# Kernel tuning notes

Measured on AMD Instinct MI355X. Metric: run time of the kernel, lower is better.

The kernel has to match this reference:

```python
import jax, jax.numpy as jnp
import numpy as np

SUBNET_NUM = 32
BATCH = 131072
H1, H2 = 10, 6          # subnet_arch = [10, 6]
SMOOTH_LAMBDA = 0.001
BN_EPS = 1e-10


def setup_inputs() -> dict:
    key = jax.random.key(0)
    ks = jax.random.split(key, 7)
    f32 = jnp.float32
    x = jax.random.normal(ks[0], (BATCH, SUBNET_NUM), f32)
    # small init scale keeps tanh in its non-saturated (smooth) regime
    W1 = 0.5 * jax.random.normal(ks[1], (SUBNET_NUM, 1, H1), f32)
    b1 = 0.1 * jax.random.normal(ks[2], (SUBNET_NUM, H1), f32)
    W2 = 0.5 * jax.random.normal(ks[3], (SUBNET_NUM, H1, H2), f32)
    b2 = 0.1 * jax.random.normal(ks[4], (SUBNET_NUM, H2), f32)
    W3 = 0.5 * jax.random.normal(ks[5], (SUBNET_NUM, H2, 1), f32)
    b3 = 0.1 * jax.random.normal(ks[6], (SUBNET_NUM, 1), f32)
    return {"x": x, "W1": W1, "b1": b1, "W2": W2, "b2": b2, "W3": W3, "b3": b3}


def _subnet_scalar(x_s, w1, b1, w2, b2, w3, b3):
    """One subnet applied to one scalar input: output and d2out/dx2."""
    def f(xs):
        h = jnp.tanh(xs * w1[0] + b1)        # [H1]  (input dim is 1)
        h = jnp.tanh(h @ w2 + b2)            # [H2]
        return (h @ w3)[0] + b3[0]           # scalar
    out = f(x_s)
    g2 = jax.grad(jax.grad(f))(x_s)          # second derivative wrt the scalar input
    return out, g2


def reference(x, W1, b1, W2, b2, W3, b3):
    # vmap over batch (inner) and over subnets (outer, axis 1 of x / axis 0 of params)
    per_batch = jax.vmap(_subnet_scalar, in_axes=(0, None, None, None, None, None, None))
    per_subnet = jax.vmap(per_batch, in_axes=(1, 0, 0, 0, 0, 0, 0), out_axes=(1, 1))
    out, g2 = per_subnet(x, W1, b1, W2, b2, W3, b3)      # each [BATCH, SUBNET_NUM]

    # BatchNorm (momentum=0.0, center=False, scale=False) in training mode:
    # normalize by batch stats; moving_variance == biased batch variance.
    mean = jnp.mean(out, axis=0)
    var = jnp.mean((out - mean) ** 2, axis=0)
    out_bn = (out - mean) * jax.lax.rsqrt(var + BN_EPS)

    # smooth penalty per subnet: mean(grad2^2) / sqrt(moving_variance)
    penalty = jnp.mean(g2 ** 2, axis=0) / jnp.sqrt(var)
    smooth_loss = SMOOTH_LAMBDA * jnp.sum(penalty)
    return out_bn, smooth_loss
```

## Files before the change

### kernel.cpp

```cpp
#include <hip/hip_runtime.h>

#define BATCH 131072
#define SN 32
#define H1 10
#define H2 6
#define TILE_ROWS 64
#define NBLK (BATCH / TILE_ROWS)
#define LDS_STRIDE 33

__device__ __forceinline__ float fast_tanh(float x) {
    float e = __expf(2.0f * x);
    float r = __builtin_amdgcn_rcpf(e + 1.0f);
    return fmaf(-2.0f, r, 1.0f);
}

__global__ __launch_bounds__(256) void k_main(
    const float* __restrict__ x,
    const float* __restrict__ W1, const float* __restrict__ B1,
    const float* __restrict__ W2, const float* __restrict__ B2,
    const float* __restrict__ W3, const float* __restrict__ B3,
    float* __restrict__ out, float* __restrict__ partial )
{
    __shared__ float xt[TILE_ROWS * LDS_STRIDE];
    const int tid = threadIdx.x;
    const int row0 = blockIdx.x * TILE_ROWS;

    const float4* xv = (const float4*)(x + (size_t)row0 * SN);
    #pragma unroll
    for (int it = 0; it < 2; ++it) {
        int v = it * 256 + tid;
        float4 val = xv[v];
        int r = v >> 3;
        int c = (v & 7) << 2;
        float* dst = &xt[r * LDS_STRIDE + c];
        dst[0] = val.x; dst[1] = val.y; dst[2] = val.z; dst[3] = val.w;
    }
    __syncthreads();

    const int lane = tid & 63;
    const int wave = tid >> 6;

    #pragma unroll 1
    for (int si = 0; si < SN / 4; ++si) {
        const int s = __builtin_amdgcn_readfirstlane(si * 4 + wave);
        const float* w1p = W1 + s * H1;
        const float* b1p = B1 + s * H1;
        const float* w2p = W2 + s * H1 * H2;
        const float* b2p = B2 + s * H2;
        const float* w3p = W3 + s * H2;
        const float b3 = B3[s];

        float w1r[H1], b1r[H1];
        #pragma unroll
        for (int i = 0; i < H1; ++i) { w1r[i] = w1p[i]; b1r[i] = b1p[i]; }
        float w2r[H1 * H2];
        #pragma unroll
        for (int k = 0; k < H1 * H2; ++k) w2r[k] = w2p[k];
        float b2r[H2], w3r[H2];
        #pragma unroll
        for (int j = 0; j < H2; ++j) { b2r[j] = b2p[j]; w3r[j] = w3p[j]; }

        const float xs = xt[lane * LDS_STRIDE + s];

        float t[H1], p[H1], q[H1];
        #pragma unroll
        for (int i = 0; i < H1; ++i) {
            float u = fmaf(xs, w1r[i], b1r[i]);
            float ti = fast_tanh(u);
            float e = fmaf(-ti, ti, 1.0f);
            t[i] = ti;
            p[i] = e * w1r[i];
            q[i] = -2.0f * ti * e * w1r[i] * w1r[i];
        }

        float outv = b3, g2 = 0.0f;
        #pragma unroll
        for (int j = 0; j < H2; ++j) {
            float v = b2r[j], a = 0.0f, c = 0.0f;
            #pragma unroll
            for (int i = 0; i < H1; ++i) {
                const float w = w2r[i * H2 + j];
                v = fmaf(w, t[i], v);
                a = fmaf(w, p[i], a);
                c = fmaf(w, q[i], c);
            }
            float sj = fast_tanh(v);
            float dj = fmaf(-sj, sj, 1.0f);
            float g2j = dj * c - 2.0f * sj * dj * a * a;
            outv = fmaf(w3r[j], sj, outv);
            g2   = fmaf(w3r[j], g2j, g2);
        }

        out[(size_t)(row0 + lane) * SN + s] = outv;

        float s1 = outv, s2 = outv * outv, s3 = g2 * g2;
        #pragma unroll
        for (int off = 32; off > 0; off >>= 1) {
            s1 += __shfl_xor(s1, off);
            s2 += __shfl_xor(s2, off);
            s3 += __shfl_xor(s3, off);
        }
        if (lane == 0) {
            partial[(size_t)(0 * SN + s) * NBLK + blockIdx.x] = s1;
            partial[(size_t)(1 * SN + s) * NBLK + blockIdx.x] = s2;
            partial[(size_t)(2 * SN + s) * NBLK + blockIdx.x] = s3;
        }
    }
}

__global__ __launch_bounds__(256) void k_reduce(const float* __restrict__ partial,
                                                double* __restrict__ acc)
{
    const float* p = partial + (size_t)blockIdx.x * NBLK;
    double s = 0.0;
    for (int i = threadIdx.x; i < NBLK; i += 256) s += (double)p[i];
    #pragma unroll
    for (int off = 32; off > 0; off >>= 1) s += __shfl_down(s, off);
    __shared__ double ws[4];
    if ((threadIdx.x & 63) == 0) ws[threadIdx.x >> 6] = s;
    __syncthreads();
    if (threadIdx.x == 0) acc[blockIdx.x] = ws[0] + ws[1] + ws[2] + ws[3];
}

__global__ __launch_bounds__(256) void k_norm(float* __restrict__ out,
                                              const double* __restrict__ acc)
{
    __shared__ float mean_s[SN], inv_s[SN];
    const int tid = threadIdx.x;
    if (tid < SN) {
        const double invB = 1.0 / (double)BATCH;
        double mean = acc[tid] * invB;
        double var = acc[SN + tid] * invB - mean * mean;
        if (var < 0.0) var = 0.0;
        mean_s[tid] = (float)mean;
        inv_s[tid] = (float)(1.0 / sqrt(var + 1e-10));
    }
    if (blockIdx.x == 0 && tid == 0) {
        const double invB = 1.0 / (double)BATCH;
        double sum = 0.0;
        for (int s = 0; s < SN; ++s) {
            double mean = acc[s] * invB;
            double var = acc[SN + s] * invB - mean * mean;
            if (var < 0.0) var = 0.0;
            sum += (acc[2 * SN + s] * invB) / sqrt(var);
        }
        out[(size_t)BATCH * SN] = (float)(0.001 * sum);
    }
    __syncthreads();
    const int v = blockIdx.x * 256 + tid;
    float4* p = (float4*)out;
    float4 val = p[v];
    const int c = (v & 7) << 2;
    val.x = (val.x - mean_s[c + 0]) * inv_s[c + 0];
    val.y = (val.y - mean_s[c + 1]) * inv_s[c + 1];
    val.z = (val.z - mean_s[c + 2]) * inv_s[c + 2];
    val.w = (val.w - mean_s[c + 3]) * inv_s[c + 3];
    p[v] = val;
}

extern "C" void kernel_launch(void* const* d_in, const int* in_sizes, int n_in,
                              void* d_out, int out_size, void* d_ws, size_t ws_size,
                              hipStream_t stream) {
    const float* x  = (const float*)d_in[0];
    const float* W1 = (const float*)d_in[1];
    const float* B1 = (const float*)d_in[2];
    const float* W2 = (const float*)d_in[3];
    const float* B2 = (const float*)d_in[4];
    const float* W3 = (const float*)d_in[5];
    const float* B3 = (const float*)d_in[6];

    float* out = (float*)d_out;
    float* partial = (float*)d_ws;
    double* acc = (double*)((char*)d_ws + (size_t)3 * SN * NBLK * sizeof(float));

    k_main<<<NBLK, 256, 0, stream>>>(x, W1, B1, W2, B2, W3, B3, out, partial);
    k_reduce<<<3 * SN, 256, 0, stream>>>(partial, acc);
    k_norm<<<(BATCH * SN / 4) / 256, 256, 0, stream>>>(out, acc);
}
```

Before: 139.5 us.

## Process two rows per lane with packed float2 math and stage outputs in LDS

Each lane now handles two batch rows using two-wide vector types, so the compiler can emit packed FP32 FMA instructions and amortize per-subnet weight loads over more rows; the tile grows to 128 rows per block. Outputs are staged in LDS and written as coalesced float4 stores instead of strided scalar stores. The second-derivative algebra is also refactored, folding the constant factor into a final multiply by 4. This adds register and LDS pressure, and the block count is halved.

```diff
diff --git a/kernel.cpp b/kernel.cpp
--- a/kernel.cpp
+++ b/kernel.cpp
@@ -4,14 +4,22 @@
 #define SN 32
 #define H1 10
 #define H2 6
-#define TILE_ROWS 64
-#define NBLK (BATCH / TILE_ROWS)
+#define ROWS 128
+#define GRID (BATCH / ROWS)
 #define LDS_STRIDE 33
 
-__device__ __forceinline__ float fast_tanh(float x) {
-    float e = __expf(2.0f * x);
-    float r = __builtin_amdgcn_rcpf(e + 1.0f);
-    return fmaf(-2.0f, r, 1.0f);
+typedef float v2f __attribute__((ext_vector_type(2)));
+
+__device__ __forceinline__ v2f bc(float s) { v2f r; r.x = s; r.y = s; return r; }
+__device__ __forceinline__ v2f fma2(v2f a, v2f b, v2f c) {
+    return __builtin_elementwise_fma(a, b, c);
+}
+__device__ __forceinline__ v2f tanh2(v2f x) {
+    v2f x2 = x + x;
+    v2f e; e.x = __expf(x2.x); e.y = __expf(x2.y);
+    v2f e1 = e + bc(1.0f);
+    v2f r; r.x = __builtin_amdgcn_rcpf(e1.x); r.y = __builtin_amdgcn_rcpf(e1.y);
+    return fma2(bc(-2.0f), r, bc(1.0f));
 }
 
 __global__ __launch_bounds__(256) void k_main(
@@ -21,13 +29,16 @@
     const float* __restrict__ W3, const float* __restrict__ B3,
     float* __restrict__ out, float* __restrict__ partial )
 {
-    __shared__ float xt[TILE_ROWS * LDS_STRIDE];
+    __shared__ float xt[ROWS * LDS_STRIDE];
+    __shared__ float ov[ROWS * LDS_STRIDE];
     const int tid = threadIdx.x;
-    const int row0 = blockIdx.x * TILE_ROWS;
-
-    const float4* xv = (const float4*)(x + (size_t)row0 * SN);
+    const int lane = tid & 63;
+    const int wave = tid >> 6;
+    const int blk = blockIdx.x;
+
+    const float4* xv = (const float4*)(x + (size_t)blk * ROWS * SN);
     #pragma unroll
-    for (int it = 0; it < 2; ++it) {
+    for (int it = 0; it < 4; ++it) {
         int v = it * 256 + tid;
         float4 val = xv[v];
         int r = v >> 3;
@@ -37,11 +48,8 @@
     }
     __syncthreads();
 
-    const int lane = tid & 63;
-    const int wave = tid >> 6;
-
     #pragma unroll 1
-    for (int si = 0; si < SN / 4; ++si) {
+    for (int si = 0; si < 8; ++si) {
         const int s = __builtin_amdgcn_readfirstlane(si * 4 + wave);
         const float* w1p = W1 + s * H1;
         const float* b1p = B1 + s * H1;
@@ -60,40 +68,49 @@
         #pragma unroll
         for (int j = 0; j < H2; ++j) { b2r[j] = b2p[j]; w3r[j] = w3p[j]; }
 
-        const float xs = xt[lane * LDS_STRIDE + s];
-
-        float t[H1], p[H1], q[H1];
+        v2f xs;
+        xs.x = xt[lane * LDS_STRIDE + s];
+        xs.y = xt[(lane + 64) * LDS_STRIDE + s];
+
+        v2f t[H1], p[H1], q[H1];
         #pragma unroll
         for (int i = 0; i < H1; ++i) {
-            float u = fmaf(xs, w1r[i], b1r[i]);
-            float ti = fast_tanh(u);
-            float e = fmaf(-ti, ti, 1.0f);
+            v2f u = fma2(xs, bc(w1r[i]), bc(b1r[i]));
+            v2f ti = tanh2(u);
+            v2f e = fma2(-ti, ti, bc(1.0f));
             t[i] = ti;
-            p[i] = e * w1r[i];
-            q[i] = -2.0f * ti * e * w1r[i] * w1r[i];
-        }
-
-        float outv = b3, g2 = 0.0f;
+            p[i] = e * bc(w1r[i]);
+            q[i] = (ti * p[i]) * bc(w1r[i]);
+        }
+
+        v2f o = bc(b3), g2a = bc(0.0f);
         #pragma unroll
         for (int j = 0; j < H2; ++j) {
-            float v = b2r[j], a = 0.0f, c = 0.0f;
+            v2f vv = bc(b2r[j]), a = bc(0.0f), c = bc(0.0f);
             #pragma unroll
             for (int i = 0; i < H1; ++i) {
-                const float w = w2r[i * H2 + j];
-                v = fmaf(w, t[i], v);
-                a = fmaf(w, p[i], a);
-                c = fmaf(w, q[i], c);
+                v2f wb = bc(w2r[i * H2 + j]);
+                vv = fma2(wb, t[i], vv);
+                a  = fma2(wb, p[i], a);
+                c  = fma2(wb, q[i], c);
             }
-            float sj = fast_tanh(v);
-            float dj = fmaf(-sj, sj, 1.0f);
-            float g2j = dj * c - 2.0f * sj * dj * a * a;
-            outv = fmaf(w3r[j], sj, outv);
-            g2   = fmaf(w3r[j], g2j, g2);
-        }
-
-        out[(size_t)(row0 + lane) * SN + s] = outv;
-
-        float s1 = outv, s2 = outv * outv, s3 = g2 * g2;
+            v2f sj = tanh2(vv);
+            v2f dj = fma2(-sj, sj, bc(1.0f));
+            v2f aa = a * a;
+            v2f h  = fma2(sj, aa, c);
+            v2f k  = dj * h;
+            o   = fma2(bc(w3r[j]), sj, o);
+            g2a = fma2(bc(w3r[j]), k, g2a);
+        }
+
+        ov[lane * LDS_STRIDE + s] = o.x;
+        ov[(lane + 64) * LDS_STRIDE + s] = o.y;
+
+        v2f s2v = o * o;
+        v2f s3v = (g2a * g2a) * bc(4.0f);
+        float s1 = o.x + o.y;
+        float s2 = s2v.x + s2v.y;
+        float s3 = s3v.x + s3v.y;
         #pragma unroll
         for (int off = 32; off > 0; off >>= 1) {
             s1 += __shfl_xor(s1, off);
@@ -101,19 +118,32 @@
             s3 += __shfl_xor(s3, off);
         }
         if (lane == 0) {
-            partial[(size_t)(0 * SN + s) * NBLK + blockIdx.x] = s1;
-            partial[(size_t)(1 * SN + s) * NBLK + blockIdx.x] = s2;
-            partial[(size_t)(2 * SN + s) * NBLK + blockIdx.x] = s3;
-        }
+            partial[(size_t)(0 * SN + s) * GRID + blk] = s1;
+            partial[(size_t)(1 * SN + s) * GRID + blk] = s2;
+            partial[(size_t)(2 * SN + s) * GRID + blk] = s3;
+        }
+    }
+    __syncthreads();
+
+    float4* po = (float4*)out;
+    const size_t base = (size_t)blk * (ROWS * SN / 4);
+    #pragma unroll
+    for (int it = 0; it < 4; ++it) {
+        int v = it * 256 + tid;
+        int r = v >> 3;
+        int c = (v & 7) << 2;
+        const float* src = &ov[r * LDS_STRIDE + c];
+        float4 w; w.x = src[0]; w.y = src[1]; w.z = src[2]; w.w = src[3];
+        po[base + v] = w;
     }
 }
 
 __global__ __launch_bounds__(256) void k_reduce(const float* __restrict__ partial,
                                                 double* __restrict__ acc)
 {
-    const float* p = partial + (size_t)blockIdx.x * NBLK;
+    const float* p = partial + (size_t)blockIdx.x * GRID;
     double s = 0.0;
-    for (int i = threadIdx.x; i < NBLK; i += 256) s += (double)p[i];
+    for (int i = threadIdx.x; i < GRID; i += 256) s += (double)p[i];
     #pragma unroll
     for (int off = 32; off > 0; off >>= 1) s += __shfl_down(s, off);
     __shared__ double ws[4];
@@ -171,9 +201,9 @@
 
     float* out = (float*)d_out;
     float* partial = (float*)d_ws;
-    double* acc = (double*)((char*)d_ws + (size_t)3 * SN * NBLK * sizeof(float));
-
-    k_main<<<NBLK, 256, 0, stream>>>(x, W1, B1, W2, B2, W3, B3, out, partial);
+    double* acc = (double*)((char*)d_ws + (size_t)3 * SN * GRID * sizeof(float));
+
+    k_main<<<GRID, 256, 0, stream>>>(x, W1, B1, W2, B2, W3, B3, out, partial);
     k_reduce<<<3 * SN, 256, 0, stream>>>(partial, acc);
     k_norm<<<(BATCH * SN / 4) / 256, 256, 0, stream>>>(out, acc);
 }
```

Measured after the change: 123.8 us. 1.13x faster.
